# Kernel tuning notes

Hardware: AMD Instinct MI355X
Metric: run time of the kernel (lower is better)

Reference implementation:

```python
import jax, jax.numpy as jnp
import numpy as np

B, T, C = 32, 512, 1024
H, D = 16, 64
BLOCK_SIZE = 512


def setup_inputs() -> dict:
    key = jax.random.key(0)
    ks = jax.random.split(key, 6)
    s_in = 1.0 / np.sqrt(C)
    return {
        "x": jax.random.normal(ks[0], (B, T, C), dtype=jnp.float32),
        "wq": jax.random.normal(ks[1], (H, C, D), dtype=jnp.float32) * s_in,
        "wk": jax.random.normal(ks[2], (H, C, D), dtype=jnp.float32) * s_in,
        "wv": jax.random.normal(ks[3], (H, C, D), dtype=jnp.float32) * s_in,
        "w_proj": jax.random.normal(ks[4], (C, C), dtype=jnp.float32) * s_in,
        "b_proj": jax.random.normal(ks[5], (C,), dtype=jnp.float32) * 0.01,
    }


def reference(x, wq, wk, wv, w_proj, b_proj):
    b, t, c = x.shape
    # per-head projections (bias=False Linears stacked on head axis)
    q = jnp.einsum("btc,hcd->bhtd", x, wq)
    k = jnp.einsum("btc,hcd->bhtd", x, wk)
    v = jnp.einsum("btc,hcd->bhtd", x, wv)
    # NOTE: original scales by 1/sqrt(C) with C = n_embd, not head_size
    scale = 1.0 / (c ** 0.5)
    scores = jnp.einsum("bhtd,bhsd->bhts", q, k) * scale  # [B,H,T,T]
    causal = jnp.tril(jnp.ones((t, t), dtype=bool))
    scores = jnp.where(causal, scores, jnp.finfo(scores.dtype).min)
    attn = jax.nn.softmax(scores, axis=-1)
    out = jnp.einsum("bhts,bhsd->bhtd", attn, v)
    # concat heads in order -> [B,T,H*D]
    out = out.transpose(0, 2, 1, 3).reshape(b, t, -1)
    # output projection (dropout = identity in eval mode)
    return out @ w_proj + b_proj
```

## Files before the change

kernel.cpp:

```cpp
#include <hip/hip_runtime.h>

typedef unsigned int u32;
typedef unsigned short u16;
typedef __bf16 bf16x8 __attribute__((ext_vector_type(8)));
typedef float f32x4 __attribute__((ext_vector_type(4)));
typedef u16 u16x8 __attribute__((ext_vector_type(8)));
typedef u16 u16x4 __attribute__((ext_vector_type(4)));

#define DEVI static __device__ __forceinline__

DEVI u16 f2bf(float f) {
  union { float f; u32 u; } v; v.f = f;
  return (u16)((v.u + 0x7fffu + ((v.u >> 16) & 1u)) >> 16);
}

DEVI u32 cvtpk(float a, float b) {
  u32 r;
  asm("v_cvt_pk_bf16_f32 %0, %1, %2" : "=v"(r) : "v"(a), "v"(b));
  return r;
}

constexpr long QS_ = 16777216;
constexpr long XB_O    = 0;
constexpr long WQKV_O  = 16777216;
constexpr long Q_O     = 19922944;
constexpr long CTX_O   = 70254592;
constexpr long WPROJ_O = 87031808;

__global__ __launch_bounds__(256) void k_cast_x(const float* __restrict__ x, u16* __restrict__ xb) {
  long i = (long)blockIdx.x * 256 + threadIdx.x;
  const float4* p = (const float4*)(x + i * 8);
  float4 a = p[0], b = p[1];
  u16x8 r;
  r[0]=f2bf(a.x); r[1]=f2bf(a.y); r[2]=f2bf(a.z); r[3]=f2bf(a.w);
  r[4]=f2bf(b.x); r[5]=f2bf(b.y); r[6]=f2bf(b.z); r[7]=f2bf(b.w);
  *(u16x8*)(xb + i * 8) = r;
}

__global__ __launch_bounds__(256) void k_prep_wqkv(const float* __restrict__ wq, const float* __restrict__ wk,
                                                   const float* __restrict__ wv, u16* __restrict__ wt) {
  long o = (long)blockIdx.x * 256 + threadIdx.x;
  int n = (int)(o >> 10), kk = (int)(o & 1023);
  int sel = n >> 10, h = (n >> 6) & 15, d = n & 63;
  const float* W = (sel == 0) ? wq : ((sel == 1) ? wk : wv);
  wt[o] = f2bf(W[((long)h * 1024 + kk) * 64 + d]);
}

__global__ __launch_bounds__(256) void k_prep_wproj(const float* __restrict__ wp, u16* __restrict__ wt) {
  long o = (long)blockIdx.x * 256 + threadIdx.x;
  int n = (int)(o >> 10), kk = (int)(o & 1023);
  wt[o] = f2bf(wp[(long)kk * 1024 + n]);
}

DEVI void gload16(const u16* g, u16* l) {
  __builtin_amdgcn_global_load_lds((const __attribute__((address_space(1))) u32*)g,
                                   (__attribute__((address_space(3))) u32*)l, 16, 0, 0);
}

template <int NN, int EPI>
__global__ __launch_bounds__(512, 2)
void k_gemm(const u16* __restrict__ A, const u16* __restrict__ Bt,
            u16* __restrict__ oq, float* __restrict__ of, const float* __restrict__ bias) {
  __shared__ u16 lds[2][4][8192];

  const int tid = threadIdx.x;
  const int lane = tid & 63;
  const int w = tid >> 6;
  const int wm = w >> 2, wn = w & 3;
  const int lg = lane >> 4, lr = lane & 15;
  const int bht = 2 + (wn >> 1);
  const int bn0 = (wn & 1) * 4;

  constexpr int NBN = NN / 256;
  const int nwg = gridDim.x;
  const int swz = ((int)blockIdx.x & 7) * (nwg >> 3) + ((int)blockIdx.x >> 3);
  const long m0 = (long)(swz / NBN) * 256, n0 = (long)(swz % NBN) * 256;

  int srcoff[2];
  #pragma unroll
  for (int r2 = 0; r2 < 2; ++r2) {
    int s = r2 * 8 + w;
    int mi = s >> 1, ks = s & 1;
    int rowl = mi * 16 + (lane >> 2);
    int colu = ks * 32 + (((lane & 3) * 8) ^ (((lane >> 5) & 1) * 16));
    srcoff[r2] = rowl * 1024 + colu;
  }
  const int fo = lr * 32 + ((lg * 8) ^ (((lr >> 3) & 1) * 16));

  const u16* At  = A  + m0 * 1024;
  const u16* Bt2 = Bt + n0 * 1024;

  f32x4 acc[8][4] = {};
  bf16x8 af[4][2];
  bf16x8 bf[4][2];

#define STAGE(buf_, ht_, gbase_)                                               \
  { _Pragma("unroll") for (int r_ = 0; r_ < 2; ++r_)                           \
      gload16((gbase_) + srcoff[r_], &lds[buf_][ht_][r_ * 4096 + w * 512]); }

#define LDS_A(buf_, milo_)                                                     \
  { _Pragma("unroll") for (int i_ = 0; i_ < 4; ++i_)                           \
    _Pragma("unroll") for (int ks_ = 0; ks_ < 2; ++ks_)                        \
      af[i_][ks_] = *(const bf16x8*)&lds[buf_][wm][((milo_ + i_) * 2 + ks_) * 512 + fo]; }

#define LDS_B(buf_, nilo_)                                                     \
  { _Pragma("unroll") for (int j_ = 0; j_ < 2; ++j_)                           \
    _Pragma("unroll") for (int ks_ = 0; ks_ < 2; ++ks_)                        \
      bf[nilo_ + j_][ks_] = *(const bf16x8*)&lds[buf_][bht][((bn0 + nilo_ + j_) * 2 + ks_) * 512 + fo]; }

#define QUAD(milo_, nilo_)                                                     \
  { __builtin_amdgcn_s_setprio(1);                                             \
    _Pragma("unroll") for (int i_ = 0; i_ < 4; ++i_)                           \
    _Pragma("unroll") for (int j_ = 0; j_ < 2; ++j_)                           \
    _Pragma("unroll") for (int ks_ = 0; ks_ < 2; ++ks_)                        \
      acc[milo_ + i_][nilo_ + j_] = __builtin_amdgcn_mfma_f32_16x16x32_bf16(   \
          af[i_][ks_], bf[nilo_ + j_][ks_], acc[milo_ + i_][nilo_ + j_], 0, 0, 0); \
    __builtin_amdgcn_s_setprio(0); }

#define WAIT_LGKM() { asm volatile("s_waitcnt lgkmcnt(0)" ::: "memory");       \
                      __builtin_amdgcn_sched_barrier(0); }

  STAGE(0, 2, Bt2);
  STAGE(0, 3, Bt2 + 131072);
  STAGE(0, 0, At);
  STAGE(0, 1, At + 131072);
  STAGE(1, 2, Bt2 + 64);
  STAGE(1, 3, Bt2 + 131072 + 64);
  asm volatile("s_waitcnt vmcnt(4)" ::: "memory");
  __builtin_amdgcn_s_barrier();

  #pragma unroll 1
  for (int t = 0; t < 16; ++t) {
    const int buf = t & 1, nbuf = buf ^ 1;
    LDS_A(buf, 0); LDS_B(buf, 0);
    if (t + 1 < 16) STAGE(nbuf, 0, At + (t + 1) * 64);
    __builtin_amdgcn_s_barrier();
    WAIT_LGKM();
    QUAD(0, 0);
    __builtin_amdgcn_s_barrier();
    LDS_B(buf, 2);
    if (t + 1 < 16) STAGE(nbuf, 1, At + 131072 + (t + 1) * 64);
    __builtin_amdgcn_s_barrier();
    WAIT_LGKM();
    QUAD(0, 2);
    __builtin_amdgcn_s_barrier();
    LDS_A(buf, 4);
    if (t + 2 < 16) STAGE(buf, 2, Bt2 + (t + 2) * 64);
    __builtin_amdgcn_s_barrier();
    WAIT_LGKM();
    QUAD(4, 2);
    __builtin_amdgcn_s_barrier();
    if (t + 2 < 16) STAGE(buf, 3, Bt2 + 131072 + (t + 2) * 64);
    __builtin_amdgcn_s_barrier();
    QUAD(4, 0);
    if (t < 14)       { asm volatile("s_waitcnt vmcnt(4)" ::: "memory"); }
    else if (t == 14) { asm volatile("s_waitcnt vmcnt(0)" ::: "memory"); }
    __builtin_amdgcn_s_barrier();
  }

  if constexpr (EPI == 0) {
    #pragma unroll
    for (int mi = 0; mi < 8; ++mi) {
      int grow = (int)m0 + wm * 128 + mi * 16 + lg * 4;
      int b = grow >> 9, t0 = grow & 511;
      #pragma unroll
      for (int ni = 0; ni < 4; ++ni) {
        int gcol = (int)n0 + wn * 64 + ni * 16 + lr;
        int sel = gcol >> 10, h = (gcol >> 6) & 15, d = gcol & 63;
        u16* dst = oq + (long)sel * QS_ + (((long)(b * 16 + h) * 512 + t0) * 64 + d);
        #pragma unroll
        for (int r = 0; r < 4; ++r) dst[r * 64] = f2bf(acc[mi][ni][r]);
      }
    }
  } else {
    float bv[4];
    #pragma unroll
    for (int ni = 0; ni < 4; ++ni) bv[ni] = bias[(int)n0 + wn * 64 + ni * 16 + lr];
    #pragma unroll
    for (int mi = 0; mi < 8; ++mi) {
      int grow = (int)m0 + wm * 128 + mi * 16 + lg * 4;
      #pragma unroll
      for (int ni = 0; ni < 4; ++ni) {
        int gcol = (int)n0 + wn * 64 + ni * 16 + lr;
        #pragma unroll
        for (int r = 0; r < 4; ++r)
          of[(long)(grow + r) * NN + gcol] = acc[mi][ni][r] + bv[ni];
      }
    }
  }
#undef STAGE
#undef LDS_A
#undef LDS_B
#undef QUAD
#undef WAIT_LGKM
}

__global__ __launch_bounds__(256, 3)
void k_attn(const u16* __restrict__ Qp, const u16* __restrict__ Kp,
            const u16* __restrict__ Vp, u16* __restrict__ ctx) {
  __shared__ u16 k_lds[2][64 * 72];
  __shared__ u16 vt_lds[2][64 * 72];

  const int bid = blockIdx.x;
  const int qi = 3 - (bid >> 9);
  const int bh = bid & 511;
  const int tid = threadIdx.x, lane = tid & 63, w = tid >> 6;
  const int lg = lane >> 4, lr = lane & 15;
  const long base = (long)bh * (512 * 64);

  const int q0 = qi * 128 + w * 32;

  bf16x8 qf[2][2];
  #pragma unroll
  for (int mt = 0; mt < 2; ++mt)
    #pragma unroll
    for (int k2 = 0; k2 < 2; ++k2)
      qf[mt][k2] = *(const bf16x8*)(Qp + base + (long)(q0 + mt * 16 + lr) * 64 + k2 * 32 + lg * 8);

  f32x4 o[2][4] = {};
  float ms[2] = {-1e30f, -1e30f};
  float ls[2] = {0.f, 0.f};

  const int nch = (qi + 1) * 2;
  int srow[2], scol[2], cslot[2];
  #pragma unroll
  for (int i = 0; i < 2; ++i) {
    int s = i * 256 + tid;
    srow[i] = s >> 3; scol[i] = s & 7;
    int sr = srow[i];
    cslot[i] = ((sr >> 5) << 5) + (((sr >> 2) & 3) << 3) + (((sr >> 4) & 1) << 2) + (sr & 3);
  }

  uint4 kreg[2], vreg[2];
  auto loadch = [&](int c) {
    #pragma unroll
    for (int i = 0; i < 2; ++i) {
      long go = base + (long)(c * 64 + srow[i]) * 64 + scol[i] * 8;
      kreg[i] = *(const uint4*)(Kp + go);
      vreg[i] = *(const uint4*)(Vp + go);
    }
  };
  auto writech = [&](int bsel) {
    #pragma unroll
    for (int i = 0; i < 2; ++i) {
      *(uint4*)&k_lds[bsel][srow[i] * 72 + scol[i] * 8] = kreg[i];
      union { uint4 v; u16 s[8]; } t; t.v = vreg[i];
      #pragma unroll
      for (int j = 0; j < 8; ++j)
        vt_lds[bsel][(scol[i] * 8 + j) * 72 + cslot[i]] = t.s[j];
    }
  };

  loadch(0);
  writech(0);
  loadch(1);
  __syncthreads();

  const float sc = 0.045084220027780106f;

  #pragma unroll 1
  for (int c = 0; c < nch; ++c) {
    const int bsel = c & 1;
    if (c + 1 < nch) writech(bsel ^ 1);
    if (c + 2 < nch) loadch(c + 2);

    if (c * 64 <= q0 + 31) {
      const bool full = (c * 64 + 63 <= q0);
      f32x4 st[2][4] = {};
      bf16x8 kf2[4][2];
      #pragma unroll
      for (int nt = 0; nt < 4; ++nt)
        #pragma unroll
        for (int k2 = 0; k2 < 2; ++k2)
          kf2[nt][k2] = *(const bf16x8*)&k_lds[bsel][(nt * 16 + lr) * 72 + k2 * 32 + lg * 8];
      #pragma unroll
      for (int mt = 0; mt < 2; ++mt)
        #pragma unroll
        for (int nt = 0; nt < 4; ++nt)
          #pragma unroll
          for (int k2 = 0; k2 < 2; ++k2)
            st[mt][nt] = __builtin_amdgcn_mfma_f32_16x16x32_bf16(kf2[nt][k2], qf[mt][k2], st[mt][nt], 0, 0, 0);

      u32 pkw[2][4][2];
      #pragma unroll
      for (int mt = 0; mt < 2; ++mt) {
        const int q = q0 + mt * 16 + lr;
        if (!full) {
          #pragma unroll
          for (int nt = 0; nt < 4; ++nt)
            #pragma unroll
            for (int r = 0; r < 4; ++r) {
              int s_ = c * 64 + nt * 16 + lg * 4 + r;
              st[mt][nt][r] = (s_ <= q) ? st[mt][nt][r] : -1e30f;
            }
        }
        float mx = st[mt][0][0];
        #pragma unroll
        for (int nt = 0; nt < 4; ++nt)
          #pragma unroll
          for (int r = 0; r < 4; ++r) mx = fmaxf(mx, st[mt][nt][r]);
        mx = fmaxf(mx, __shfl_xor(mx, 16));
        mx = fmaxf(mx, __shfl_xor(mx, 32));
        const float mnew = fmaxf(ms[mt], mx);
        const float alpha = exp2f((ms[mt] - mnew) * sc);
        ms[mt] = mnew;
        const float msc = mnew * sc;
        float ps = 0.f;
        float p[4][4];
        #pragma unroll
        for (int nt = 0; nt < 4; ++nt)
          #pragma unroll
          for (int r = 0; r < 4; ++r) {
            float pv = exp2f(fmaf(st[mt][nt][r], sc, -msc));
            p[nt][r] = pv;
            ps += pv;
          }
        ps += __shfl_xor(ps, 16);
        ps += __shfl_xor(ps, 32);
        ls[mt] = ls[mt] * alpha + ps;
        #pragma unroll
        for (int nt = 0; nt < 4; ++nt) {
          pkw[mt][nt][0] = cvtpk(p[nt][0], p[nt][1]);
          pkw[mt][nt][1] = cvtpk(p[nt][2], p[nt][3]);
        }
        #pragma unroll
        for (int dt = 0; dt < 4; ++dt) o[mt][dt] *= alpha;
      }

      bf16x8 vf2[4][2];
      #pragma unroll
      for (int dt = 0; dt < 4; ++dt)
        #pragma unroll
        for (int k2 = 0; k2 < 2; ++k2)
          vf2[dt][k2] = *(const bf16x8*)&vt_lds[bsel][(dt * 16 + lr) * 72 + k2 * 32 + lg * 8];
      #pragma unroll
      for (int mt = 0; mt < 2; ++mt)
        #pragma unroll
        for (int k2 = 0; k2 < 2; ++k2) {
          union { u32 w4[4]; bf16x8 v; } pb;
          pb.w4[0] = pkw[mt][2 * k2][0];
          pb.w4[1] = pkw[mt][2 * k2][1];
          pb.w4[2] = pkw[mt][2 * k2 + 1][0];
          pb.w4[3] = pkw[mt][2 * k2 + 1][1];
          #pragma unroll
          for (int dt = 0; dt < 4; ++dt)
            o[mt][dt] = __builtin_amdgcn_mfma_f32_16x16x32_bf16(vf2[dt][k2], pb.v, o[mt][dt], 0, 0, 0);
        }
    }
    __syncthreads();
  }

  const int b = bh >> 4, h = bh & 15;
  #pragma unroll
  for (int mt = 0; mt < 2; ++mt) {
    const int t = q0 + mt * 16 + lr;
    const float inv = 1.0f / ls[mt];
    #pragma unroll
    for (int dt = 0; dt < 4; ++dt) {
      u16x4 pk4;
      #pragma unroll
      for (int r = 0; r < 4; ++r) pk4[r] = f2bf(o[mt][dt][r] * inv);
      *(u16x4*)(ctx + ((long)(b * 512 + t)) * 1024 + h * 64 + dt * 16 + lg * 4) = pk4;
    }
  }
}

extern "C" void kernel_launch(void* const* d_in, const int* in_sizes, int n_in,
                              void* d_out, int out_size, void* d_ws, size_t ws_size,
                              hipStream_t stream) {
  const float* x  = (const float*)d_in[0];
  const float* wq = (const float*)d_in[1];
  const float* wk = (const float*)d_in[2];
  const float* wv = (const float*)d_in[3];
  const float* wp = (const float*)d_in[4];
  const float* bp = (const float*)d_in[5];
  float* out = (float*)d_out;
  u16* ws = (u16*)d_ws;

  u16* XB    = ws + XB_O;
  u16* WQKV  = ws + WQKV_O;
  u16* Qb    = ws + Q_O;
  u16* CTX   = ws + CTX_O;
  u16* WPROJ = ws + WPROJ_O;

  k_cast_x<<<8192, 256, 0, stream>>>(x, XB);
  k_prep_wqkv<<<12288, 256, 0, stream>>>(wq, wk, wv, WQKV);
  k_prep_wproj<<<4096, 256, 0, stream>>>(wp, WPROJ);
  k_gemm<3072, 0><<<(16384 / 256) * (3072 / 256), 512, 0, stream>>>(XB, WQKV, Qb, nullptr, nullptr);
  k_attn<<<2048, 256, 0, stream>>>(Qb, Qb + QS_, Qb + 2 * QS_, CTX);
  k_gemm<1024, 1><<<(16384 / 256) * (1024 / 256), 512, 0, stream>>>(CTX, WPROJ, nullptr, out, bp);
}
```

Measured before the change: 252.3 us.

## Stage GEMM epilogues through LDS for vectorized stores; raise priority around attention MFMAs

Both GEMM epilogues now write accumulators into a padded shared-memory tile, then read them back as contiguous rows. This lets each thread emit 16-byte stores: bf16x8 for the QKV scatter and float4 plus bias for the projection output, replacing scattered 2-byte and 4-byte stores. The shared buffer grows to 67584 u16 so it can hold a padded 256x264 bf16 tile, which adds LDS footprint and extra barriers. Separately, the attention kernel wraps its MFMA blocks in s_setprio(1)/s_setprio(0) to favour waves issuing matrix ops.

```diff
diff --git a/kernel.cpp b/kernel.cpp
--- a/kernel.cpp
+++ b/kernel.cpp
@@ -61,7 +61,8 @@
 __global__ __launch_bounds__(512, 2)
 void k_gemm(const u16* __restrict__ A, const u16* __restrict__ Bt,
             u16* __restrict__ oq, float* __restrict__ of, const float* __restrict__ bias) {
-  __shared__ u16 lds[2][4][8192];
+  __shared__ __align__(16) u16 smem[67584];
+  u16 (*lds)[4][8192] = reinterpret_cast<u16(*)[4][8192]>(smem);
 
   const int tid = threadIdx.x;
   const int lane = tid & 63;
@@ -159,32 +160,58 @@
   }
 
   if constexpr (EPI == 0) {
+    __syncthreads();
+    u16* T = smem;
     #pragma unroll
     for (int mi = 0; mi < 8; ++mi) {
-      int grow = (int)m0 + wm * 128 + mi * 16 + lg * 4;
+      int rl0 = wm * 128 + mi * 16 + lg * 4;
+      #pragma unroll
+      for (int ni = 0; ni < 4; ++ni) {
+        int cl = wn * 64 + ni * 16 + lr;
+        #pragma unroll
+        for (int r = 0; r < 4; ++r)
+          T[(rl0 + r) * 264 + cl] = f2bf(acc[mi][ni][r]);
+      }
+    }
+    __syncthreads();
+    const int col16 = tid & 31;
+    #pragma unroll
+    for (int jj = 0; jj < 16; ++jj) {
+      int row = jj * 16 + (tid >> 5);
+      u16x8 v = *(const u16x8*)&T[row * 264 + col16 * 8];
+      int grow = (int)m0 + row;
       int b = grow >> 9, t0 = grow & 511;
-      #pragma unroll
-      for (int ni = 0; ni < 4; ++ni) {
-        int gcol = (int)n0 + wn * 64 + ni * 16 + lr;
-        int sel = gcol >> 10, h = (gcol >> 6) & 15, d = gcol & 63;
-        u16* dst = oq + (long)sel * QS_ + (((long)(b * 16 + h) * 512 + t0) * 64 + d);
-        #pragma unroll
-        for (int r = 0; r < 4; ++r) dst[r * 64] = f2bf(acc[mi][ni][r]);
+      int gcol = (int)n0 + col16 * 8;
+      int sel = gcol >> 10, h = (gcol >> 6) & 15, d = gcol & 63;
+      *(u16x8*)(oq + (long)sel * QS_ + (((long)(b * 16 + h) * 512 + t0) * 64 + d)) = v;
+    }
+  } else {
+    float* Tf = (float*)smem;
+    const int col4 = tid & 63;
+    float4 bv4 = *(const float4*)&bias[(int)n0 + col4 * 4];
+    #pragma unroll
+    for (int half = 0; half < 2; ++half) {
+      __syncthreads();
+      #pragma unroll
+      for (int mi = 0; mi < 4; ++mi) {
+        int rl0 = wm * 64 + mi * 16 + lg * 4;
+        #pragma unroll
+        for (int ni = 0; ni < 4; ++ni) {
+          int cl = wn * 64 + ni * 16 + lr;
+          #pragma unroll
+          for (int r = 0; r < 4; ++r)
+            Tf[(rl0 + r) * 264 + cl] = acc[half * 4 + mi][ni][r];
+        }
       }
-    }
-  } else {
-    float bv[4];
-    #pragma unroll
-    for (int ni = 0; ni < 4; ++ni) bv[ni] = bias[(int)n0 + wn * 64 + ni * 16 + lr];
-    #pragma unroll
-    for (int mi = 0; mi < 8; ++mi) {
-      int grow = (int)m0 + wm * 128 + mi * 16 + lg * 4;
-      #pragma unroll
-      for (int ni = 0; ni < 4; ++ni) {
-        int gcol = (int)n0 + wn * 64 + ni * 16 + lr;
-        #pragma unroll
-        for (int r = 0; r < 4; ++r)
-          of[(long)(grow + r) * NN + gcol] = acc[mi][ni][r] + bv[ni];
+      __syncthreads();
+      #pragma unroll
+      for (int jj = 0; jj < 16; ++jj) {
+        int rloc = jj * 8 + (tid >> 6);
+        float4 v = *(const float4*)&Tf[rloc * 264 + col4 * 4];
+        v.x += bv4.x; v.y += bv4.y; v.z += bv4.z; v.w += bv4.w;
+        int wmr = rloc >> 6, inner = rloc & 63;
+        int grow = (int)m0 + wmr * 128 + half * 64 + inner;
+        *(float4*)(of + (long)grow * NN + (int)n0 + col4 * 4) = v;
       }
     }
   }
@@ -273,6 +300,7 @@
         #pragma unroll
         for (int k2 = 0; k2 < 2; ++k2)
           kf2[nt][k2] = *(const bf16x8*)&k_lds[bsel][(nt * 16 + lr) * 72 + k2 * 32 + lg * 8];
+      __builtin_amdgcn_s_setprio(1);
       #pragma unroll
       for (int mt = 0; mt < 2; ++mt)
         #pragma unroll
@@ -280,6 +308,7 @@
           #pragma unroll
           for (int k2 = 0; k2 < 2; ++k2)
             st[mt][nt] = __builtin_amdgcn_mfma_f32_16x16x32_bf16(kf2[nt][k2], qf[mt][k2], st[mt][nt], 0, 0, 0);
+      __builtin_amdgcn_s_setprio(0);
 
       u32 pkw[2][4][2];
       #pragma unroll
@@ -333,6 +362,7 @@
         #pragma unroll
         for (int k2 = 0; k2 < 2; ++k2)
           vf2[dt][k2] = *(const bf16x8*)&vt_lds[bsel][(dt * 16 + lr) * 72 + k2 * 32 + lg * 8];
+      __builtin_amdgcn_s_setprio(1);
       #pragma unroll
       for (int mt = 0; mt < 2; ++mt)
         #pragma unroll
@@ -346,6 +376,7 @@
           for (int dt = 0; dt < 4; ++dt)
             o[mt][dt] = __builtin_amdgcn_mfma_f32_16x16x32_bf16(vf2[dt][k2], pb.v, o[mt][dt], 0, 0, 0);
         }
+      __builtin_amdgcn_s_setprio(0);
     }
     __syncthreads();
   }
```

Measured after the change: 256.2 us. No clear change (+1.5%).
